# Kernel optimization log

Measured on AMD Instinct MI355X. Metric: run time of the kernel, lower is better.

Reference implementation:

```python
import jax, jax.numpy as jnp
import numpy as np

NT, NC = 100000, 25000
ETT, ECT = 800000, 400000
DIN_T, DIN_C = 64, 32
H, C = 4, 32
HID = H * C  # 128
SLOPE = 0.2  # GATConv LeakyReLU negative slope


def setup_inputs() -> dict:
    key = jax.random.key(0)
    ks = jax.random.split(key, 24)
    def p(i, shape, s=0.05):
        return jax.random.normal(ks[i], shape, dtype=jnp.float32) * s
    return {
        'x_target': jax.random.normal(ks[0], (NT, DIN_T), dtype=jnp.float32),
        'x_context': jax.random.normal(ks[1], (NC, DIN_C), dtype=jnp.float32),
        'edge_tt': jax.random.randint(ks[2], (2, ETT), 0, NT),
        'edge_ct_src': jax.random.randint(ks[3], (ECT,), 0, NC),
        'edge_ct_dst': jax.random.randint(ks[4], (ECT,), 0, NT),
        'W_pre_t': p(5, (DIN_T, HID)), 'b_pre_t': jnp.zeros((HID,), jnp.float32),
        'W_pre_c': p(6, (DIN_C, HID)), 'b_pre_c': jnp.zeros((HID,), jnp.float32),
        'W_sd': p(7, (HID, HID)), 'att_src_sd': p(8, (H, C)), 'att_dst_sd': p(9, (H, C)), 'b_sd': jnp.zeros((HID,), jnp.float32),
        'W_ds': p(10, (HID, HID)), 'att_src_ds': p(11, (H, C)), 'att_dst_ds': p(12, (H, C)), 'b_ds': jnp.zeros((HID,), jnp.float32),
        'W_ct_src': p(13, (HID, HID)), 'W_ct_dst': p(14, (HID, HID)), 'att_src_ct': p(15, (H, C)), 'att_dst_ct': p(16, (H, C)), 'b_ct': jnp.zeros((HID,), jnp.float32),
        'W_out': p(17, (HID, HID)), 'b_out': jnp.zeros((HID,), jnp.float32),
    }


def _gat(h_src, h_dst, att_s, att_d, src, dst, n_dst, bias):
    # h_src: [N_src,H,C] transformed src feats; h_dst: [N_dst,H,C]
    a_s = jnp.einsum('nhc,hc->nh', h_src, att_s)  # [N_src,H]
    a_d = jnp.einsum('nhc,hc->nh', h_dst, att_d)  # [N_dst,H]
    e = a_s[src] + a_d[dst]                        # [E,H]
    e = jnp.where(e > 0, e, SLOPE * e)             # LeakyReLU(0.2)
    m = jax.ops.segment_max(e, dst, num_segments=n_dst)  # stable softmax per dst
    ex = jnp.exp(e - m[dst])
    den = jax.ops.segment_sum(ex, dst, num_segments=n_dst)
    alpha = ex / den[dst]                          # [E,H]
    msg = h_src[src] * alpha[:, :, None]           # [E,H,C]
    out = jax.ops.segment_sum(msg, dst, num_segments=n_dst)
    return out.reshape(n_dst, H * C) + bias


def reference(x_target, x_context, edge_tt, edge_ct_src, edge_ct_dst,
              W_pre_t, b_pre_t, W_pre_c, b_pre_c,
              W_sd, att_src_sd, att_dst_sd, b_sd,
              W_ds, att_src_ds, att_dst_ds, b_ds,
              W_ct_src, W_ct_dst, att_src_ct, att_dst_ct, b_ct,
              W_out, b_out):
    # HeteroDictLinear pretransform + relu
    h_t = jax.nn.relu(x_target @ W_pre_t + b_pre_t)   # [NT,128]
    h_c = jax.nn.relu(x_context @ W_pre_c + b_pre_c)  # [NC,128]
    res = h_t
    # DirGATConv on (target,to,target): forward + reversed, each w/ self-loops
    loops = jnp.arange(NT)
    src_f = jnp.concatenate([edge_tt[0], loops]); dst_f = jnp.concatenate([edge_tt[1], loops])
    src_r = jnp.concatenate([edge_tt[1], loops]); dst_r = jnp.concatenate([edge_tt[0], loops])
    hs = (h_t @ W_sd).reshape(NT, H, C)
    out_sd = _gat(hs, hs, att_src_sd, att_dst_sd, src_f, dst_f, NT, b_sd)
    hd = (h_t @ W_ds).reshape(NT, H, C)
    out_ds = _gat(hd, hd, att_src_ds, att_dst_ds, src_r, dst_r, NT, b_ds)
    out_tt = 0.5 * out_sd + 0.5 * out_ds  # (1-alpha), alpha with alpha=0.5
    # bipartite GATConv on (context,to,target), no self loops
    hcs = (h_c @ W_ct_src).reshape(NC, H, C)
    htd = (h_t @ W_ct_dst).reshape(NT, H, C)
    out_ct = _gat(hcs, htd, att_src_ct, att_dst_ct, edge_ct_src, edge_ct_dst, NT, b_ct)
    # HeteroConv aggr='mean' over the two edge types hitting 'target'
    x = 0.5 * (out_tt + out_ct)
    x = jax.nn.relu(x + res)  # skip connection + relu
    return x @ W_out + b_out
```

## Files before the change

### kernel.cpp

```cpp
#include <hip/hip_runtime.h>
#include <cstdint>
#include <cstddef>

typedef unsigned short u16;
typedef unsigned int u32;

#define NT 100000
#define NC 25000
#define ETT 800000
#define ECT 400000
#define SLOPE 0.2f
#define LOG2E 1.4426950408889634f
#define OFFS (NT + 4)

#define NBK 782
#define NBLK 256
#define CHT ((ETT + NBLK - 1) / NBLK)
#define CHC ((ECT + NBLK - 1) / NBLK)
#define TOTC (3 * NBK * NBLK)
#define NSB ((TOTC + 4095) / 4096)
#define FILL_CAP 4096

#define PT_BLK ((NT + 63) / 64)
#define CT_BLK ((NC + 63) / 64)

typedef __attribute__((ext_vector_type(8))) short bf16x8;
typedef __attribute__((ext_vector_type(4))) float f32x4;

__device__ __forceinline__ u16 f2bf(float f) {
  u32 u = __float_as_uint(f);
  u32 r = (u >> 16) & 1u;
  return (u16)((u + 0x7fffu + r) >> 16);
}
__device__ __forceinline__ float lof(u32 p) { return __uint_as_float(p << 16); }
__device__ __forceinline__ float hif(u32 p) { return __uint_as_float(p & 0xffff0000u); }

__device__ __forceinline__ void compute_bpre(const int* __restrict__ bsum, int* s_bpre) {
  const int t = threadIdx.x;
  const int v = (t < NSB) ? bsum[t] : 0;
  s_bpre[t] = v;
  __syncthreads();
  for (int d = 1; d < 256; d <<= 1) {
    const int u = (t >= d) ? s_bpre[t - d] : 0;
    __syncthreads();
    s_bpre[t] += u;
    __syncthreads();
  }
  const int incl = s_bpre[t];
  __syncthreads();
  s_bpre[t] = incl - v;
  __syncthreads();
}

__global__ __launch_bounds__(256) void transform_hist_kernel(
    const int* __restrict__ tt_src, const int* __restrict__ tt_dst,
    const int* __restrict__ ect_d, int* __restrict__ cntblk,
    const float* __restrict__ Wsd, const float* __restrict__ AsSd, const float* __restrict__ AdSd,
    const float* __restrict__ Wds, const float* __restrict__ AsDs, const float* __restrict__ AdDs,
    const float* __restrict__ Wout,
    u16* __restrict__ bf_sd, u16* __restrict__ bf_ds, u16* __restrict__ bf_out,
    const float* __restrict__ Wcd, const float* __restrict__ attD,
    const float* __restrict__ bsd, const float* __restrict__ bds, const float* __restrict__ bct,
    float* __restrict__ cbias,
    const float* __restrict__ x_t, const float* __restrict__ Wpt, const float* __restrict__ bpt,
    u16* __restrict__ h_t, float* __restrict__ aD,
    const float* __restrict__ x_c, const float* __restrict__ Wpc, const float* __restrict__ bpc,
    const float* __restrict__ Wcs, const float* __restrict__ attS,
    u16* __restrict__ hc_bf, float* __restrict__ aS_c)
{
  __shared__ __align__(16) char smem[51200];
  const int t = threadIdx.x;

  if (blockIdx.x < NBLK) {
    int* h = (int*)smem;
    const int b = blockIdx.x;
    for (int i = t; i < 3 * NBK; i += 256) h[i] = 0;
    __syncthreads();
    const int lo = b * CHT, hi = min(lo + CHT, ETT);
    for (int i = lo + t; i < hi; i += 256) {
      atomicAdd(&h[tt_dst[i] >> 7], 1);
      atomicAdd(&h[NBK + (tt_src[i] >> 7)], 1);
    }
    const int lo2 = b * CHC, hi2 = min(lo2 + CHC, ECT);
    for (int i = lo2 + t; i < hi2; i += 256)
      atomicAdd(&h[2 * NBK + (ect_d[i] >> 7)], 1);
    __syncthreads();
    for (int i = t; i < 3 * NBK; i += 256)
      cntblk[(size_t)i * NBLK + b] = h[i];
    return;
  }

  const int b = blockIdx.x - NBLK;

  if (b < 4) {
    if (b == 3) {
      if (t < 128) cbias[t] = 0.25f * bsd[t] + 0.25f * bds[t] + 0.5f * bct[t];
      return;
    }
    float* fS = (float*)smem;
    float* fD = fS + 512;
    const float* W = (b == 0) ? Wsd : (b == 1) ? Wds : Wout;
    const float* As = (b == 0) ? AsSd : AsDs;
    const float* Ad = (b == 0) ? AdSd : AdDs;
    u16* out = (b == 0) ? bf_sd : (b == 1) ? bf_ds : bf_out;
    const int tiles = (b == 2) ? 8 : 9;
    if (b < 2) {
      if (t < 128) {
        for (int hh = 0; hh < 4; ++hh) {
          float s1 = 0.f, s2 = 0.f;
          for (int c = 0; c < 32; ++c) {
            const float wv = W[t * 128 + hh * 32 + c];
            s1 = fmaf(wv, As[hh * 32 + c], s1);
            s2 = fmaf(wv, Ad[hh * 32 + c], s2);
          }
          fS[t * 4 + hh] = s1 * LOG2E; fD[t * 4 + hh] = s2 * LOG2E;
        }
      }
      __syncthreads();
    }
    const int total = tiles * 4 * 64 * 8;
    for (int i = t; i < total; i += 256) {
// ... 34 lines not shown
    }
    const int rg = t >> 4;
    const int cg = t & 15;
    float acc[4][8];
    for (int r = 0; r < 4; ++r)
      for (int j = 0; j < 8; ++j)
        acc[r][j] = bpt[cg * 4 + (j & 3) + (j >> 2) * 64];
    for (int kc = 0; kc < 64; kc += 32) {
      for (int j = 0; j < 4; ++j) {
        const int idx = t + j * 256;
        const int k = idx >> 5, c4 = (idx & 31) * 4;
        *(float4*)&s_W[k][c4] = *(const float4*)(Wpt + (size_t)(kc + k) * 128 + c4);
      }
      __syncthreads();
#pragma unroll 8
      for (int k = 0; k < 32; ++k) {
        const float4 xa = *(const float4*)&s_xt[kc + k][rg * 4];
        const float4 w0 = *(const float4*)&s_W[k][cg * 4];
        const float4 w1 = *(const float4*)&s_W[k][cg * 4 + 64];
        const float xr[4] = {xa.x, xa.y, xa.z, xa.w};
        for (int r = 0; r < 4; ++r) {
          acc[r][0] = fmaf(xr[r], w0.x, acc[r][0]);
          acc[r][1] = fmaf(xr[r], w0.y, acc[r][1]);
          acc[r][2] = fmaf(xr[r], w0.z, acc[r][2]);
          acc[r][3] = fmaf(xr[r], w0.w, acc[r][3]);
          acc[r][4] = fmaf(xr[r], w1.x, acc[r][4]);
          acc[r][5] = fmaf(xr[r], w1.y, acc[r][5]);
          acc[r][6] = fmaf(xr[r], w1.z, acc[r][6]);
          acc[r][7] = fmaf(xr[r], w1.w, acc[r][7]);
        }
      }
      __syncthreads();
    }
    float4 fc0[2], fc1[2];
    fc0[0] = *(const float4*)&s_fold[(cg * 4 + 0) * 4];
    (void)fc0; (void)fc1;
    for (int r = 0; r < 4; ++r) {
      const int grow = row0 + rg * 4 + r;
      float v[8];
      for (int j = 0; j < 8; ++j) v[j] = fmaxf(acc[r][j], 0.f);
      float p0 = 0.f, p1 = 0.f, p2 = 0.f, p3 = 0.f;
      for (int j = 0; j < 8; ++j) {
        const int col = cg * 4 + (j & 3) + ((j >> 2) * 64);
        const float4 f4 = *(const float4*)&s_fold[col * 4];
        p0 = fmaf(v[j], f4.x, p0); p1 = fmaf(v[j], f4.y, p1);
        p2 = fmaf(v[j], f4.z, p2); p3 = fmaf(v[j], f4.w, p3);
      }
      if (grow < NT) {
        uint2 pk;
        pk.x = (u32)f2bf(v[0]) | ((u32)f2bf(v[1]) << 16);
        pk.y = (u32)f2bf(v[2]) | ((u32)f2bf(v[3]) << 16);
        *(uint2*)(h_t + (size_t)grow * 128 + cg * 4) = pk;
        pk.x = (u32)f2bf(v[4]) | ((u32)f2bf(v[5]) << 16);
        pk.y = (u32)f2bf(v[6]) | ((u32)f2bf(v[7]) << 16);
        *(uint2*)(h_t + (size_t)grow * 128 + cg * 4 + 64) = pk;
      }
      for (int m = 1; m < 16; m <<= 1) {
        p0 += __shfl_xor(p0, m); p1 += __shfl_xor(p1, m);
        p2 += __shfl_xor(p2, m); p3 += __shfl_xor(p3, m);
      }
      if (cg == 0 && grow < NT)
        *(float4*)(aD + (size_t)grow * 4) = make_float4(p0, p1, p2, p3);
    }
    return;
  }

  {
    float (*s_ht)[68]  = (float(*)[68])smem;
    float (*s_W2)[128] = (float(*)[128])(smem + 34816);
// ... 81 lines not shown
        __syncthreads();
      }
    }
    const int h2 = cg >> 3;
    const float4 at0 = *(const float4*)(attS + cg * 4);
    const float4 at1 = *(const float4*)(attS + cg * 4 + 64);
    for (int r = 0; r < 4; ++r) {
      const int grow = row0 + rg * 4 + r;
      float pa = acc2[r][0] * at0.x + acc2[r][1] * at0.y +
                 acc2[r][2] * at0.z + acc2[r][3] * at0.w;
      float pb = acc2[r][4] * at1.x + acc2[r][5] * at1.y +
                 acc2[r][6] * at1.z + acc2[r][7] * at1.w;
      if (grow < NC) {
        uint2 pk;
        pk.x = (u32)f2bf(acc2[r][0]) | ((u32)f2bf(acc2[r][1]) << 16);
        pk.y = (u32)f2bf(acc2[r][2]) | ((u32)f2bf(acc2[r][3]) << 16);
        *(uint2*)(hc_bf + (size_t)grow * 128 + cg * 4) = pk;
        pk.x = (u32)f2bf(acc2[r][4]) | ((u32)f2bf(acc2[r][5]) << 16);
        pk.y = (u32)f2bf(acc2[r][6]) | ((u32)f2bf(acc2[r][7]) << 16);
        *(uint2*)(hc_bf + (size_t)grow * 128 + cg * 4 + 64) = pk;
      }
      for (int m = 1; m < 8; m <<= 1) {
        pa += __shfl_xor(pa, m);
        pb += __shfl_xor(pb, m);
      }
      if ((cg & 7) == 0 && grow < NC) {
        aS_c[(size_t)grow * 4 + h2] = pa * LOG2E;
        aS_c[(size_t)grow * 4 + 2 + h2] = pb * LOG2E;
      }
    }
  }
}

__global__ __launch_bounds__(256) void scan2_blk_kernel(const int* __restrict__ in,
    int* __restrict__ out, int* __restrict__ bsum)
{
  const int t = threadIdx.x, b = blockIdx.x;
  const int idx = b * 4096 + t * 16;
  int v[16];
  int s = 0;
  if (idx < TOTC) {
#pragma unroll
    for (int q = 0; q < 4; ++q) {
      const int4 qq = *(const int4*)(in + idx + q * 4);
      v[q * 4 + 0] = s; s += qq.x;
      v[q * 4 + 1] = s; s += qq.y;
      v[q * 4 + 2] = s; s += qq.z;
      v[q * 4 + 3] = s; s += qq.w;
    }
  } else {
    for (int j = 0; j < 16; ++j) v[j] = 0;
  }
  __shared__ int sh[256];
  sh[t] = s;
  __syncthreads();
  for (int d = 1; d < 256; d <<= 1) {
    const int u = (t >= d) ? sh[t - d] : 0;
    __syncthreads();
    sh[t] += u;
    __syncthreads();
  }
  const int excl = (t == 0) ? 0 : sh[t - 1];
  if (idx < TOTC) {
#pragma unroll
    for (int q = 0; q < 4; ++q) {
      int4 qo;
      qo.x = excl + v[q * 4 + 0]; qo.y = excl + v[q * 4 + 1];
      qo.z = excl + v[q * 4 + 2]; qo.w = excl + v[q * 4 + 3];
      *(int4*)(out + idx + q * 4) = qo;
    }
  }
  if (t == 255) bsum[b] = sh[255];
}

__global__ __launch_bounds__(256) void bin_logits2_kernel(
    const int* __restrict__ tt_src, const int* __restrict__ tt_dst,
    const int* __restrict__ ect_s, const int* __restrict__ ect_d,
    const int* __restrict__ scanned, const int* __restrict__ bsum, u32* __restrict__ bin,
    const short* __restrict__ A, const short* __restrict__ Bsd, const short* __restrict__ Bds,
    u16* __restrict__ hs, float* __restrict__ aSsd, float* __restrict__ aDsd,
    u16* __restrict__ hd, float* __restrict__ aSds, float* __restrict__ aDds, int M)
{
  __shared__ __align__(16) float ldsf[4][16][148];
  const int t = threadIdx.x;

  if (blockIdx.x < NBLK) {
    int* cur = (int*)&ldsf[0][0][0];
    int* s_bpre = cur + 3 * NBK;
    compute_bpre(bsum, s_bpre);
    const int b = blockIdx.x;
    for (int i = t; i < 3 * NBK; i += 256) {
      const int idx = i * NBLK + b;
      cur[i] = scanned[idx] + s_bpre[idx >> 12];
    }
    __syncthreads();
    const int lo = b * CHT, hi = min(lo + CHT, ETT);
    for (int i = lo + t; i < hi; i += 256) {
      const int s = tt_src[i], d = tt_dst[i];
      int p = atomicAdd(&cur[d >> 7], 1);
      bin[p] = ((u32)(d & 127) << 17) | (u32)s;
      p = atomicAdd(&cur[NBK + (s >> 7)], 1);
      bin[p] = ((u32)(s & 127) << 17) | (u32)d;
    }
    const int lo2 = b * CHC, hi2 = min(lo2 + CHC, ECT);
    for (int i = lo2 + t; i < hi2; i += 256) {
      const int s = ect_s[i], d = ect_d[i];
      const int p = atomicAdd(&cur[2 * NBK + (d >> 7)], 1);
      bin[p] = ((u32)(d & 127) << 17) | (u32)s;
    }
    return;
  }

  float (*lds)[16][148] = ldsf;
  const int blk = blockIdx.x - NBLK;
  const int wv = t >> 6, lane = t & 63;
  const int quad = lane >> 4, l16 = lane & 15;
  const int row0 = blk * 64 + wv * 16;
  const int arow = min(row0 + l16, M - 1);
  const short* ap = A + (size_t)arow * 128 + quad * 8;
  bf16x8 af[4];
  for (int ks = 0; ks < 4; ++ks) af[ks] = *(const bf16x8*)(ap + ks * 32);
  const int row = row0 + l16;
  const int idx = lane & 7, rr = lane >> 3;
  for (int pass = 0; pass < 2; ++pass) {
    const short* B = pass ? Bds : Bsd;
    u16* outb = pass ? hd : hs;
    float* aS = pass ? aSds : aSsd;
    float* aD = pass ? aDds : aDsd;
    f32x4 acc[9];
    for (int ti = 0; ti < 9; ++ti) acc[ti] = (f32x4){0.f, 0.f, 0.f, 0.f};
    for (int ks = 0; ks < 4; ++ks)
      for (int ti = 0; ti < 9; ++ti) {
        const bf16x8 bf = *(const bf16x8*)(B + ((ti * 4 + ks) * 64 + lane) * 8);
        acc[ti] = __builtin_amdgcn_mfma_f32_16x16x32_bf16(af[ks], bf, acc[ti], 0, 0, 0);
      }
    for (int ti = 0; ti < 9; ++ti)
      for (int r = 0; r < 4; ++r)
        lds[wv][quad * 4 + r][ti * 16 + l16] = acc[ti][r];
    __syncthreads();
    if (row < M) {
      for (int g = 0; g < 8; ++g) {
        const f32x4 v = *(const f32x4*)&lds[wv][l16][g * 16 + quad * 4];
        uint2 pk;
        pk.x = (u32)f2bf(v[0]) | ((u32)f2bf(v[1]) << 16);
        pk.y = (u32)f2bf(v[2]) | ((u32)f2bf(v[3]) << 16);
        *(uint2*)(outb + (size_t)row * 128 + g * 16 + quad * 4) = pk;
      }
    }
    for (int p = 0; p < 2; ++p) {
      const int lr = p * 8 + rr;
      const int n = row0 + lr;
      if (n < M) {
        const float v = lds[wv][lr][128 + idx];
        if (idx < 4) aS[(size_t)n * 4 + idx] = v;
        else aD[(size_t)n * 4 + idx - 4] = v;
      }
    }
    __syncthreads();
  }
}

__global__ __launch_bounds__(256) void bucket_fill_kernel(const int* __restrict__ scanned,
    const int* __restrict__ bsum, const u32* __restrict__ bin,
    int* __restrict__ offs, int* __restrict__ big_el)
{
  __shared__ int s_cnt[128], s_exc[128], s_cur[128], s_bpre[256];
  __shared__ int s_el[FILL_CAP];
  const int t = threadIdx.x;
  compute_bpre(bsum, s_bpre);
  const int rel = blockIdx.x / NBK;
  const int bucket = blockIdx.x - rel * NBK;
  if (t < 128) s_cnt[t] = 0;
  const int bi = blockIdx.x * NBLK;
  const int base = scanned[bi] + s_bpre[bi >> 12];
  const int nxt = (blockIdx.x == 3 * NBK - 1)
                      ? (2 * ETT + ECT)
                      : scanned[bi + NBLK] + s_bpre[(bi + NBLK) >> 12];
  __syncthreads();
  const int size = nxt - base;
  for (int i = t; i < size; i += 256)
    atomicAdd(&s_cnt[bin[base + i] >> 17], 1);
  __syncthreads();
  if (t < 128) s_exc[t] = s_cnt[t];
  __syncthreads();
  for (int d = 1; d < 128; d <<= 1) {
    int v = 0;
    if (t < 128 && t >= d) v = s_exc[t - d];
    __syncthreads();
    if (t < 128) s_exc[t] += v;
    __syncthreads();
  }
  const int relbase = rel * ETT;
  const int obase = base - relbase;
  int* off_rel = offs + (size_t)rel * OFFS;
  const int node0 = bucket * 128;
  if (t < 128) {
    const int excl = s_exc[t] - s_cnt[t];
    s_cur[t] = excl;
    if (node0 + t < NT) off_rel[node0 + t] = obase + excl;
  }
  if (t == 0 && bucket == NBK - 1) off_rel[NT] = obase + size;
  __syncthreads();
  int* el_rel = big_el + relbase;
  if (size <= FILL_CAP) {
    for (int i = t; i < size; i += 256) {
      const u32 e = bin[base + i];
      const int pos = atomicAdd(&s_cur[e >> 17], 1);
      s_el[pos] = (int)(e & 0x1FFFFu);
    }
    __syncthreads();
    for (int i = t; i < size; i += 256)
      el_rel[obase + i] = s_el[i];
  } else {
    for (int i = t; i < size; i += 256) {
      const u32 e = bin[base + i];
      const int pos = atomicAdd(&s_cur[e >> 17], 1);
      el_rel[obase + pos] = (int)(e & 0x1FFFFu);
    }
  }
}

__global__ __launch_bounds__(256) void mfma_out_kernel(
    const short* __restrict__ A, const short* __restrict__ B,
    const float* __restrict__ bias, float* __restrict__ out, int M)
{
  __shared__ __align__(16) float lds[4][16][132];
  const int wv = threadIdx.x >> 6, lane = threadIdx.x & 63;
  const int quad = lane >> 4, l16 = lane & 15;
  const int row0 = blockIdx.x * 64 + wv * 16;
  const int arow = min(row0 + l16, M - 1);
  const short* ap = A + (size_t)arow * 128 + quad * 8;
  bf16x8 af[4];
  for (int ks = 0; ks < 4; ++ks) af[ks] = *(const bf16x8*)(ap + ks * 32);
  f32x4 acc[8];
  for (int t = 0; t < 8; ++t) acc[t] = (f32x4){0.f, 0.f, 0.f, 0.f};
  for (int ks = 0; ks < 4; ++ks)
    for (int t = 0; t < 8; ++t) {
      const bf16x8 bf = *(const bf16x8*)(B + ((t * 4 + ks) * 64 + lane) * 8);
      acc[t] = __builtin_amdgcn_mfma_f32_16x16x32_bf16(af[ks], bf, acc[t], 0, 0, 0);
    }
  for (int t = 0; t < 8; ++t)
    for (int r = 0; r < 4; ++r)
      lds[wv][quad * 4 + r][t * 16 + l16] = acc[t][r];
  __syncthreads();
  const int row = row0 + l16;
  if (row < M) {
    for (int g = 0; g < 8; ++g) {
      const int col = g * 16 + quad * 4;
      f32x4 v = *(const f32x4*)&lds[wv][l16][col];
      const f32x4 b4 = *(const f32x4*)(bias + col);
      v = v + b4;
      *(f32x4*)(out + (size_t)row * 128 + col) = v;
    }
  }
}

__device__ __forceinline__ void gat_pipe16(const int* __restrict__ off,
    const int* __restrict__ el, const float* __restrict__ aS, const float* __restrict__ aD,
    const u16* __restrict__ hb, int d, int h, int cb, int self_loop, float w,
    float* __restrict__ acc)
{
  const float ad = aD[(size_t)d * 4 + h];
  const int beg = off[d];
  const int m = off[d + 1] - beg;
  const int cnt = m + self_loop;
  if (cnt <= 0) return;
  float den = 0.f;
  float a0 = 0.f, a1 = 0.f, a2 = 0.f, a3 = 0.f, a4 = 0.f, a5 = 0.f, a6 = 0.f, a7 = 0.f;
  int sB = (1 < m) ? el[beg + 1] : d;
  {
    const int sA0 = (0 < m) ? el[beg] : d;
    float eA = aS[(size_t)sA0 * 4 + h];
    uint4 pA = *(const uint4*)(hb + (size_t)sA0 * 128 + cb);
    for (int k = 0; k < cnt; ++k) {
      const int sC = (k + 2 < m) ? el[beg + k + 2] : d;
      const float eB = aS[(size_t)sB * 4 + h];
      const uint4 pB = *(const uint4*)(hb + (size_t)sB * 128 + cb);
      float ea = eA + ad;
      ea = ea > 0.f ? ea : SLOPE * ea;
      const float ex = exp2f(ea);
      den += ex;
      a0 = fmaf(ex, lof(pA.x), a0); a1 = fmaf(ex, hif(pA.x), a1);
      a2 = fmaf(ex, lof(pA.y), a2); a3 = fmaf(ex, hif(pA.y), a3);
      a4 = fmaf(ex, lof(pA.z), a4); a5 = fmaf(ex, hif(pA.z), a5);
      a6 = fmaf(ex, lof(pA.w), a6); a7 = fmaf(ex, hif(pA.w), a7);
      eA = eB; pA = pB; sB = sC;
    }
  }
  const float s = w / den;
  acc[0] = fmaf(a0, s, acc[0]); acc[1] = fmaf(a1, s, acc[1]);
  acc[2] = fmaf(a2, s, acc[2]); acc[3] = fmaf(a3, s, acc[3]);
  acc[4] = fmaf(a4, s, acc[4]); acc[5] = fmaf(a5, s, acc[5]);
  acc[6] = fmaf(a6, s, acc[6]); acc[7] = fmaf(a7, s, acc[7]);
}

__global__ __launch_bounds__(256) void gather_all_kernel(
    const int* __restrict__ off_f, const int* __restrict__ el_f,
    const float* __restrict__ aS_sd, const float* __restrict__ aD_sd, const u16* __restrict__ hs,
    const int* __restrict__ off_r, const int* __restrict__ el_r,
    const float* __restrict__ aS_ds, const float* __restrict__ aD_ds, const u16* __restrict__ hd,
    const int* __restrict__ off_c, const int* __restrict__ el_c,
    const float* __restrict__ aS_ct, const float* __restrict__ aD_ct, const u16* __restrict__ hc,
    const u16* __restrict__ skip, const float* __restrict__ cbias, u16* __restrict__ x)
{
  const int d = blockIdx.x * 16 + (threadIdx.x >> 4);
  if (d >= NT) return;
  const int lg = threadIdx.x & 15;
  const int h = lg >> 2;
  const int cb = lg * 8;
  float acc[8];
  for (int i = 0; i < 8; ++i) acc[i] = 0.f;
  gat_pipe16(off_f, el_f, aS_sd, aD_sd, hs, d, h, cb, 1, 0.25f, acc);
  gat_pipe16(off_r, el_r, aS_ds, aD_ds, hd, d, h, cb, 1, 0.25f, acc);
  gat_pipe16(off_c, el_c, aS_ct, aD_ct, hc, d, h, cb, 0, 0.5f, acc);
  const uint4 sk = *(const uint4*)(skip + (size_t)d * 128 + cb);
  const float4 cb0 = *(const float4*)(cbias + cb);
  const float4 cb1 = *(const float4*)(cbias + cb + 4);
  const float o0 = fmaxf(acc[0] + cb0.x + lof(sk.x), 0.f);
  const float o1 = fmaxf(acc[1] + cb0.y + hif(sk.x), 0.f);
  const float o2 = fmaxf(acc[2] + cb0.z + lof(sk.y), 0.f);
  const float o3 = fmaxf(acc[3] + cb0.w + hif(sk.y), 0.f);
  const float o4 = fmaxf(acc[4] + cb1.x + lof(sk.z), 0.f);
  const float o5 = fmaxf(acc[5] + cb1.y + hif(sk.z), 0.f);
  const float o6 = fmaxf(acc[6] + cb1.z + lof(sk.w), 0.f);
  const float o7 = fmaxf(acc[7] + cb1.w + hif(sk.w), 0.f);
  uint4 r;
  r.x = (u32)f2bf(o0) | ((u32)f2bf(o1) << 16);
  r.y = (u32)f2bf(o2) | ((u32)f2bf(o3) << 16);
  r.z = (u32)f2bf(o4) | ((u32)f2bf(o5) << 16);
  r.w = (u32)f2bf(o6) | ((u32)f2bf(o7) << 16);
  *(uint4*)(x + (size_t)d * 128 + cb) = r;
}

extern "C" void kernel_launch(void* const* d_in, const int* in_sizes, int n_in,
                              void* d_out, int out_size, void* d_ws, size_t ws_size,
                              hipStream_t stream)
{
  const float* x_t   = (const float*)d_in[0];
  const float* x_c   = (const float*)d_in[1];
  const int*   e_tt  = (const int*)d_in[2];
  const int*   ect_s = (const int*)d_in[3];
  const int*   ect_d = (const int*)d_in[4];
  const float* Wpt = (const float*)d_in[5];   const float* bpt = (const float*)d_in[6];
  const float* Wpc = (const float*)d_in[7];   const float* bpc = (const float*)d_in[8];
  const float* Wsd = (const float*)d_in[9];   const float* As_sd = (const float*)d_in[10];
  const float* Ad_sd = (const float*)d_in[11]; const float* bsd = (const float*)d_in[12];
  const float* Wds = (const float*)d_in[13];  const float* As_ds = (const float*)d_in[14];
  const float* Ad_ds = (const float*)d_in[15]; const float* bds = (const float*)d_in[16];
  const float* Wcs = (const float*)d_in[17];  const float* Wcd = (const float*)d_in[18];
  const float* As_ct = (const float*)d_in[19]; const float* Ad_ct = (const float*)d_in[20];
  const float* bct = (const float*)d_in[21];
  const float* Wout = (const float*)d_in[22]; const float* bout = (const float*)d_in[23];

  char* p = (char*)d_ws;
  size_t off = 0;
  auto alloc = [&](size_t bytes) { char* r = p + off; off += (bytes + 255) & ~(size_t)255; return r; };
  u16* ht_bf   = (u16*)alloc((size_t)NT * 128 * 2);
  u16* hs_bf   = (u16*)alloc((size_t)NT * 128 * 2);
  u16* hd_bf   = (u16*)alloc((size_t)NT * 128 * 2);
  u16* hc_bf   = (u16*)alloc((size_t)NC * 128 * 2);
  u16* x_bf    = (u16*)alloc((size_t)NT * 128 * 2);
  float* aS_sd = (float*)alloc((size_t)NT * 4 * 4);
  float* aD_sd = (float*)alloc((size_t)NT * 4 * 4);
  float* aS_ds = (float*)alloc((size_t)NT * 4 * 4);
  float* aD_ds = (float*)alloc((size_t)NT * 4 * 4);
  float* aS_ct = (float*)alloc((size_t)NC * 4 * 4);
  float* aD_ct = (float*)alloc((size_t)NT * 4 * 4);
  int* cntblk  = (int*)alloc((size_t)TOTC * 4);
  int* scanned = (int*)alloc((size_t)TOTC * 4);
  u32* bin     = (u32*)alloc((size_t)(2 * ETT + ECT) * 4);
  int* big_el  = (int*)alloc((size_t)(2 * ETT + ECT) * 4);
  int* offs    = (int*)alloc((size_t)3 * OFFS * 4);
  int* bsum    = (int*)alloc((size_t)NSB * 4);
  float* cbias   = (float*)alloc(128 * 4);
  u16* bfrag_sd  = (u16*)alloc((size_t)9 * 4 * 64 * 8 * 2);
  u16* bfrag_ds  = (u16*)alloc((size_t)9 * 4 * 64 * 8 * 2);
  u16* bfrag_out = (u16*)alloc((size_t)8 * 4 * 64 * 8 * 2);

  int* off_f = offs;
  int* off_r = offs + OFFS;
  int* off_c = offs + 2 * OFFS;
  int* el_f = big_el;
  int* el_r = big_el + ETT;
  int* el_c = big_el + 2 * ETT;

  const int* tt_src = e_tt;
  const int* tt_dst = e_tt + ETT;

  const int gM = (NT + 63) / 64;

  transform_hist_kernel<<<NBLK + 4 + PT_BLK + CT_BLK, 256, 0, stream>>>(
      tt_src, tt_dst, ect_d, cntblk,
      Wsd, As_sd, Ad_sd, Wds, As_ds, Ad_ds, Wout,
      bfrag_sd, bfrag_ds, bfrag_out,
      Wcd, Ad_ct, bsd, bds, bct, cbias,
      x_t, Wpt, bpt, ht_bf, aD_ct,
      x_c, Wpc, bpc, Wcs, As_ct, hc_bf, aS_ct);

  scan2_blk_kernel<<<NSB, 256, 0, stream>>>(cntblk, scanned, bsum);

  bin_logits2_kernel<<<NBLK + gM, 256, 0, stream>>>(
      tt_src, tt_dst, ect_s, ect_d, scanned, bsum, bin,
      (const short*)ht_bf, (const short*)bfrag_sd, (const short*)bfrag_ds,
      hs_bf, aS_sd, aD_sd, hd_bf, aS_ds, aD_ds, NT);

  bucket_fill_kernel<<<3 * NBK, 256, 0, stream>>>(scanned, bsum, bin, offs, big_el);

  gather_all_kernel<<<(NT + 15) / 16, 256, 0, stream>>>(
      off_f, el_f, aS_sd, aD_sd, hs_bf,
      off_r, el_r, aS_ds, aD_ds, hd_bf,
      off_c, el_c, aS_ct, aD_ct, hc_bf,
      ht_bf, cbias, x_bf);

  mfma_out_kernel<<<gM, 256, 0, stream>>>((const short*)x_bf, (const short*)bfrag_out,
                                          bout, (float*)d_out, NT);
}
```

Before: 375.7 us.

## Replace bucketed two-pass CSR build with per-node degree count and direct scatter

The old CSR build did a per-block bucket histogram, a scan, a binning pass and a separate bucket_fill kernel that sorted each bucket in LDS. The new build counts per-node degree with global atomics, scans the node offsets and scatters edge ids straight into the CSR array using atomic cursors. This drops one kernel launch and the intermediate bin buffer, so the edge data is written once instead of twice. In exchange it relies on contended global atomics on random node addresses, needs an extra memset, and the order of edges within a node becomes nondeterministic.

```diff
diff --git a/kernel.cpp b/kernel.cpp
--- a/kernel.cpp
+++ b/kernel.cpp
@@ -13,13 +13,12 @@
 #define LOG2E 1.4426950408889634f
 #define OFFS (NT + 4)
 
-#define NBK 782
 #define NBLK 256
 #define CHT ((ETT + NBLK - 1) / NBLK)
 #define CHC ((ECT + NBLK - 1) / NBLK)
-#define TOTC (3 * NBK * NBLK)
-#define NSB ((TOTC + 4095) / 4096)
-#define FILL_CAP 4096
+#define NSB2 74
+#define SCN (NSB2 * 4096)
+#define PER (SCN / NBLK)
 
 #define PT_BLK ((NT + 63) / 64)
 #define CT_BLK ((NC + 63) / 64)
@@ -35,9 +34,10 @@
 __device__ __forceinline__ float lof(u32 p) { return __uint_as_float(p << 16); }
 __device__ __forceinline__ float hif(u32 p) { return __uint_as_float(p & 0xffff0000u); }
 
-__device__ __forceinline__ void compute_bpre(const int* __restrict__ bsum, int* s_bpre) {
+__device__ __forceinline__ void compute_bpre(const int* __restrict__ bsum,
+                                             int* s_bpre, int n) {
   const int t = threadIdx.x;
-  const int v = (t < NSB) ? bsum[t] : 0;
+  const int v = (t < n) ? bsum[t] : 0;
   s_bpre[t] = v;
   __syncthreads();
   for (int d = 1; d < 256; d <<= 1) {
@@ -52,9 +52,9 @@
   __syncthreads();
 }
 
-__global__ __launch_bounds__(256) void transform_hist_kernel(
+__global__ __launch_bounds__(256) void transform_count_kernel(
     const int* __restrict__ tt_src, const int* __restrict__ tt_dst,
-    const int* __restrict__ ect_d, int* __restrict__ cntblk,
+    const int* __restrict__ ect_d, int* __restrict__ deg,
     const float* __restrict__ Wsd, const float* __restrict__ AsSd, const float* __restrict__ AdSd,
     const float* __restrict__ Wds, const float* __restrict__ AsDs, const float* __restrict__ AdDs,
     const float* __restrict__ Wout,
@@ -72,21 +72,15 @@
   const int t = threadIdx.x;
 
   if (blockIdx.x < NBLK) {
-    int* h = (int*)smem;
     const int b = blockIdx.x;
-    for (int i = t; i < 3 * NBK; i += 256) h[i] = 0;
-    __syncthreads();
     const int lo = b * CHT, hi = min(lo + CHT, ETT);
     for (int i = lo + t; i < hi; i += 256) {
-      atomicAdd(&h[tt_dst[i] >> 7], 1);
-      atomicAdd(&h[NBK + (tt_src[i] >> 7)], 1);
+      atomicAdd(&deg[tt_dst[i]], 1);
+      atomicAdd(&deg[OFFS + tt_src[i]], 1);
     }
     const int lo2 = b * CHC, hi2 = min(lo2 + CHC, ECT);
     for (int i = lo2 + t; i < hi2; i += 256)
-      atomicAdd(&h[2 * NBK + (ect_d[i] >> 7)], 1);
-    __syncthreads();
-    for (int i = t; i < 3 * NBK; i += 256)
-      cntblk[(size_t)i * NBLK + b] = h[i];
+      atomicAdd(&deg[2 * OFFS + ect_d[i]], 1);
     return;
   }
 
@@ -187,9 +181,6 @@
       }
       __syncthreads();
     }
-    float4 fc0[2], fc1[2];
-    fc0[0] = *(const float4*)&s_fold[(cg * 4 + 0) * 4];
-    (void)fc0; (void)fc1;
     for (int r = 0; r < 4; ++r) {
       const int grow = row0 + rg * 4 + r;
       float v[8];
@@ -337,24 +328,20 @@
   }
 }
 
-__global__ __launch_bounds__(256) void scan2_blk_kernel(const int* __restrict__ in,
-    int* __restrict__ out, int* __restrict__ bsum)
+__global__ __launch_bounds__(256) void scan_nodes_kernel(const int* __restrict__ deg,
+    int* __restrict__ offs, int* __restrict__ cur, int* __restrict__ bsum)
 {
   const int t = threadIdx.x, b = blockIdx.x;
   const int idx = b * 4096 + t * 16;
   int v[16];
   int s = 0;
-  if (idx < TOTC) {
 #pragma unroll
-    for (int q = 0; q < 4; ++q) {
-      const int4 qq = *(const int4*)(in + idx + q * 4);
-      v[q * 4 + 0] = s; s += qq.x;
-      v[q * 4 + 1] = s; s += qq.y;
-      v[q * 4 + 2] = s; s += qq.z;
-      v[q * 4 + 3] = s; s += qq.w;
-    }
-  } else {
-    for (int j = 0; j < 16; ++j) v[j] = 0;
+  for (int q = 0; q < 4; ++q) {
+    const int4 qq = *(const int4*)(deg + idx + q * 4);
+    v[q * 4 + 0] = s; s += qq.x;
+    v[q * 4 + 1] = s; s += qq.y;
+    v[q * 4 + 2] = s; s += qq.z;
+    v[q * 4 + 3] = s; s += qq.w;
   }
   __shared__ int sh[256];
   sh[t] = s;
@@ -366,22 +353,22 @@
     __syncthreads();
   }
   const int excl = (t == 0) ? 0 : sh[t - 1];
-  if (idx < TOTC) {
 #pragma unroll
-    for (int q = 0; q < 4; ++q) {
-      int4 qo;
-      qo.x = excl + v[q * 4 + 0]; qo.y = excl + v[q * 4 + 1];
-      qo.z = excl + v[q * 4 + 2]; qo.w = excl + v[q * 4 + 3];
-      *(int4*)(out + idx + q * 4) = qo;
-    }
+  for (int q = 0; q < 4; ++q) {
+    int4 qo;
+    qo.x = excl + v[q * 4 + 0]; qo.y = excl + v[q * 4 + 1];
+    qo.z = excl + v[q * 4 + 2]; qo.w = excl + v[q * 4 + 3];
+    *(int4*)(offs + idx + q * 4) = qo;
+    *(int4*)(cur + idx + q * 4) = qo;
   }
   if (t == 255) bsum[b] = sh[255];
 }
 
-__global__ __launch_bounds__(256) void bin_logits2_kernel(
+__global__ __launch_bounds__(256) void scatter_logits2_kernel(
     const int* __restrict__ tt_src, const int* __restrict__ tt_dst,
     const int* __restrict__ ect_s, const int* __restrict__ ect_d,
-    const int* __restrict__ scanned, const int* __restrict__ bsum, u32* __restrict__ bin,
+    int* __restrict__ offs, int* __restrict__ cur, const int* __restrict__ bsum,
+    int* __restrict__ big_el,
     const short* __restrict__ A, const short* __restrict__ Bsd, const short* __restrict__ Bds,
     u16* __restrict__ hs, float* __restrict__ aSsd, float* __restrict__ aDsd,
     u16* __restrict__ hd, float* __restrict__ aSds, float* __restrict__ aDds, int M)
@@ -390,28 +377,26 @@
   const int t = threadIdx.x;
 
   if (blockIdx.x < NBLK) {
-    int* cur = (int*)&ldsf[0][0][0];
-    int* s_bpre = cur + 3 * NBK;
-    compute_bpre(bsum, s_bpre);
+    int* s_bpre = (int*)&ldsf[0][0][0];
+    compute_bpre(bsum, s_bpre, NSB2);
     const int b = blockIdx.x;
-    for (int i = t; i < 3 * NBK; i += 256) {
-      const int idx = i * NBLK + b;
-      cur[i] = scanned[idx] + s_bpre[idx >> 12];
-    }
-    __syncthreads();
+    for (int i = t; i < PER; i += 256) {
+      const int idx = b * PER + i;
+      offs[idx] += s_bpre[idx >> 12];
+    }
     const int lo = b * CHT, hi = min(lo + CHT, ETT);
     for (int i = lo + t; i < hi; i += 256) {
       const int s = tt_src[i], d = tt_dst[i];
-      int p = atomicAdd(&cur[d >> 7], 1);
-      bin[p] = ((u32)(d & 127) << 17) | (u32)s;
-      p = atomicAdd(&cur[NBK + (s >> 7)], 1);
-      bin[p] = ((u32)(s & 127) << 17) | (u32)d;
+      int p = atomicAdd(&cur[d], 1) + s_bpre[d >> 12];
+      big_el[p] = s;
+      p = atomicAdd(&cur[OFFS + s], 1) + s_bpre[(OFFS + s) >> 12];
+      big_el[p] = d;
     }
     const int lo2 = b * CHC, hi2 = min(lo2 + CHC, ECT);
     for (int i = lo2 + t; i < hi2; i += 256) {
-      const int s = ect_s[i], d = ect_d[i];
-      const int p = atomicAdd(&cur[2 * NBK + (d >> 7)], 1);
-      bin[p] = ((u32)(d & 127) << 17) | (u32)s;
+      const int dd = ect_d[i];
+      const int p = atomicAdd(&cur[2 * OFFS + dd], 1) + s_bpre[(2 * OFFS + dd) >> 12];
+      big_el[p] = ect_s[i];
     }
     return;
   }
@@ -462,66 +447,6 @@
       }
     }
     __syncthreads();
-  }
-}
-
-__global__ __launch_bounds__(256) void bucket_fill_kernel(const int* __restrict__ scanned,
-    const int* __restrict__ bsum, const u32* __restrict__ bin,
-    int* __restrict__ offs, int* __restrict__ big_el)
-{
-  __shared__ int s_cnt[128], s_exc[128], s_cur[128], s_bpre[256];
-  __shared__ int s_el[FILL_CAP];
-  const int t = threadIdx.x;
-  compute_bpre(bsum, s_bpre);
-  const int rel = blockIdx.x / NBK;
-  const int bucket = blockIdx.x - rel * NBK;
-  if (t < 128) s_cnt[t] = 0;
-  const int bi = blockIdx.x * NBLK;
-  const int base = scanned[bi] + s_bpre[bi >> 12];
-  const int nxt = (blockIdx.x == 3 * NBK - 1)
-                      ? (2 * ETT + ECT)
-                      : scanned[bi + NBLK] + s_bpre[(bi + NBLK) >> 12];
-  __syncthreads();
-  const int size = nxt - base;
-  for (int i = t; i < size; i += 256)
-    atomicAdd(&s_cnt[bin[base + i] >> 17], 1);
-  __syncthreads();
-  if (t < 128) s_exc[t] = s_cnt[t];
-  __syncthreads();
-  for (int d = 1; d < 128; d <<= 1) {
-    int v = 0;
-    if (t < 128 && t >= d) v = s_exc[t - d];
-    __syncthreads();
-    if (t < 128) s_exc[t] += v;
-    __syncthreads();
-  }
-  const int relbase = rel * ETT;
-  const int obase = base - relbase;
-  int* off_rel = offs + (size_t)rel * OFFS;
-  const int node0 = bucket * 128;
-  if (t < 128) {
-    const int excl = s_exc[t] - s_cnt[t];
-    s_cur[t] = excl;
-    if (node0 + t < NT) off_rel[node0 + t] = obase + excl;
-  }
-  if (t == 0 && bucket == NBK - 1) off_rel[NT] = obase + size;
-  __syncthreads();
-  int* el_rel = big_el + relbase;
-  if (size <= FILL_CAP) {
-    for (int i = t; i < size; i += 256) {
-      const u32 e = bin[base + i];
-      const int pos = atomicAdd(&s_cur[e >> 17], 1);
-      s_el[pos] = (int)(e & 0x1FFFFu);
-    }
-    __syncthreads();
-    for (int i = t; i < size; i += 256)
-      el_rel[obase + i] = s_el[i];
-  } else {
-    for (int i = t; i < size; i += 256) {
-      const u32 e = bin[base + i];
-      const int pos = atomicAdd(&s_cur[e >> 17], 1);
-      el_rel[obase + pos] = (int)(e & 0x1FFFFu);
-    }
   }
 }
 
@@ -671,50 +596,42 @@
   float* aD_ds = (float*)alloc((size_t)NT * 4 * 4);
   float* aS_ct = (float*)alloc((size_t)NC * 4 * 4);
   float* aD_ct = (float*)alloc((size_t)NT * 4 * 4);
-  int* cntblk  = (int*)alloc((size_t)TOTC * 4);
-  int* scanned = (int*)alloc((size_t)TOTC * 4);
-  u32* bin     = (u32*)alloc((size_t)(2 * ETT + ECT) * 4);
+  int* deg     = (int*)alloc((size_t)SCN * 4);
+  int* offs    = (int*)alloc((size_t)SCN * 4);
+  int* cur     = (int*)alloc((size_t)SCN * 4);
   int* big_el  = (int*)alloc((size_t)(2 * ETT + ECT) * 4);
-  int* offs    = (int*)alloc((size_t)3 * OFFS * 4);
-  int* bsum    = (int*)alloc((size_t)NSB * 4);
+  int* bsum    = (int*)alloc((size_t)NSB2 * 4);
   float* cbias   = (float*)alloc(128 * 4);
   u16* bfrag_sd  = (u16*)alloc((size_t)9 * 4 * 64 * 8 * 2);
   u16* bfrag_ds  = (u16*)alloc((size_t)9 * 4 * 64 * 8 * 2);
   u16* bfrag_out = (u16*)alloc((size_t)8 * 4 * 64 * 8 * 2);
 
-  int* off_f = offs;
-  int* off_r = offs + OFFS;
-  int* off_c = offs + 2 * OFFS;
-  int* el_f = big_el;
-  int* el_r = big_el + ETT;
-  int* el_c = big_el + 2 * ETT;
-
   const int* tt_src = e_tt;
   const int* tt_dst = e_tt + ETT;
 
   const int gM = (NT + 63) / 64;
 
-  transform_hist_kernel<<<NBLK + 4 + PT_BLK + CT_BLK, 256, 0, stream>>>(
-      tt_src, tt_dst, ect_d, cntblk,
+  hipMemsetAsync(deg, 0, (size_t)SCN * 4, stream);
+
+  transform_count_kernel<<<NBLK + 4 + PT_BLK + CT_BLK, 256, 0, stream>>>(
+      tt_src, tt_dst, ect_d, deg,
       Wsd, As_sd, Ad_sd, Wds, As_ds, Ad_ds, Wout,
       bfrag_sd, bfrag_ds, bfrag_out,
       Wcd, Ad_ct, bsd, bds, bct, cbias,
       x_t, Wpt, bpt, ht_bf, aD_ct,
       x_c, Wpc, bpc, Wcs, As_ct, hc_bf, aS_ct);
 
-  scan2_blk_kernel<<<NSB, 256, 0, stream>>>(cntblk, scanned, bsum);
-
-  bin_logits2_kernel<<<NBLK + gM, 256, 0, stream>>>(
-      tt_src, tt_dst, ect_s, ect_d, scanned, bsum, bin,
+  scan_nodes_kernel<<<NSB2, 256, 0, stream>>>(deg, offs, cur, bsum);
+
+  scatter_logits2_kernel<<<NBLK + gM, 256, 0, stream>>>(
+      tt_src, tt_dst, ect_s, ect_d, offs, cur, bsum, big_el,
       (const short*)ht_bf, (const short*)bfrag_sd, (const short*)bfrag_ds,
       hs_bf, aS_sd, aD_sd, hd_bf, aS_ds, aD_ds, NT);
 
-  bucket_fill_kernel<<<3 * NBK, 256, 0, stream>>>(scanned, bsum, bin, offs, big_el);
-
   gather_all_kernel<<<(NT + 15) / 16, 256, 0, stream>>>(
-      off_f, el_f, aS_sd, aD_sd, hs_bf,
-      off_r, el_r, aS_ds, aD_ds, hd_bf,
-      off_c, el_c, aS_ct, aD_ct, hc_bf,
+      offs, big_el, aS_sd, aD_sd, hs_bf,
+      offs + OFFS, big_el, aS_ds, aD_ds, hd_bf,
+      offs + 2 * OFFS, big_el, aS_ct, aD_ct, hc_bf,
       ht_bf, cbias, x_bf);
 
   mfma_out_kernel<<<gM, 256, 0, stream>>>((const short*)x_bf, (const short*)bfrag_out,
```

Measured after the change: 496.9 us. 32.3% more time.

## Split logits and output GEMM across kernels to overlap with fill and gather

Applied to the files above, without the earlier changes.

The logits MFMA work is split in half: the first half still runs alongside edge binning, and the second half now shares a launch with the bucket-fill blocks. The gather is also split at a row boundary. The second gather half runs in the same launch as the output GEMM for the first half of rows, and a final small kernel handles the remaining output rows. The intent is to fill idle CUs during the memory-bound and atomic-heavy phases with independent compute, cutting tail effects and launch gaps. The cost is extra kernel-body complexity, and co-resident blocks of different kinds may contend for LDS and occupancy.

```diff
diff --git a/kernel.cpp b/kernel.cpp
--- a/kernel.cpp
+++ b/kernel.cpp
@@ -23,6 +23,14 @@
 
 #define PT_BLK ((NT + 63) / 64)
 #define CT_BLK ((NC + 63) / 64)
+
+#define LROWS1 782
+#define LROWS2 781
+#define GOH 50048
+#define G1BLK (GOH / 16)
+#define G2BLK ((NT - GOH + 15) / 16)
+#define OB1 (GOH / 64)
+#define OB2 ((NT - GOH + 63) / 64)
 
 typedef __attribute__((ext_vector_type(8))) short bf16x8;
 typedef __attribute__((ext_vector_type(4))) float f32x4;
@@ -187,9 +195,6 @@
       }
       __syncthreads();
     }
-    float4 fc0[2], fc1[2];
-    fc0[0] = *(const float4*)&s_fold[(cg * 4 + 0) * 4];
-    (void)fc0; (void)fc1;
     for (int r = 0; r < 4; ++r) {
       const int grow = row0 + rg * 4 + r;
       float v[8];
@@ -378,49 +383,15 @@
   if (t == 255) bsum[b] = sh[255];
 }
 
-__global__ __launch_bounds__(256) void bin_logits2_kernel(
-    const int* __restrict__ tt_src, const int* __restrict__ tt_dst,
-    const int* __restrict__ ect_s, const int* __restrict__ ect_d,
-    const int* __restrict__ scanned, const int* __restrict__ bsum, u32* __restrict__ bin,
+__device__ __forceinline__ void logits2_body(float (*lds)[16][148], int blk, int rbase,
     const short* __restrict__ A, const short* __restrict__ Bsd, const short* __restrict__ Bds,
     u16* __restrict__ hs, float* __restrict__ aSsd, float* __restrict__ aDsd,
     u16* __restrict__ hd, float* __restrict__ aSds, float* __restrict__ aDds, int M)
 {
-  __shared__ __align__(16) float ldsf[4][16][148];
   const int t = threadIdx.x;
-
-  if (blockIdx.x < NBLK) {
-    int* cur = (int*)&ldsf[0][0][0];
-    int* s_bpre = cur + 3 * NBK;
-    compute_bpre(bsum, s_bpre);
-    const int b = blockIdx.x;
-    for (int i = t; i < 3 * NBK; i += 256) {
-      const int idx = i * NBLK + b;
-      cur[i] = scanned[idx] + s_bpre[idx >> 12];
-    }
-    __syncthreads();
-    const int lo = b * CHT, hi = min(lo + CHT, ETT);
-    for (int i = lo + t; i < hi; i += 256) {
-      const int s = tt_src[i], d = tt_dst[i];
-      int p = atomicAdd(&cur[d >> 7], 1);
-      bin[p] = ((u32)(d & 127) << 17) | (u32)s;
-      p = atomicAdd(&cur[NBK + (s >> 7)], 1);
-      bin[p] = ((u32)(s & 127) << 17) | (u32)d;
-    }
-    const int lo2 = b * CHC, hi2 = min(lo2 + CHC, ECT);
-    for (int i = lo2 + t; i < hi2; i += 256) {
-      const int s = ect_s[i], d = ect_d[i];
-      const int p = atomicAdd(&cur[2 * NBK + (d >> 7)], 1);
-      bin[p] = ((u32)(d & 127) << 17) | (u32)s;
-    }
-    return;
-  }
-
-  float (*lds)[16][148] = ldsf;
-  const int blk = blockIdx.x - NBLK;
   const int wv = t >> 6, lane = t & 63;
   const int quad = lane >> 4, l16 = lane & 15;
-  const int row0 = blk * 64 + wv * 16;
+  const int row0 = rbase + blk * 64 + wv * 16;
   const int arow = min(row0 + l16, M - 1);
   const short* ap = A + (size_t)arow * 128 + quad * 8;
   bf16x8 af[4];
@@ -465,90 +436,145 @@
   }
 }
 
-__global__ __launch_bounds__(256) void bucket_fill_kernel(const int* __restrict__ scanned,
-    const int* __restrict__ bsum, const u32* __restrict__ bin,
-    int* __restrict__ offs, int* __restrict__ big_el)
-{
-  __shared__ int s_cnt[128], s_exc[128], s_cur[128], s_bpre[256];
-  __shared__ int s_el[FILL_CAP];
+__global__ __launch_bounds__(256) void bin_logits2_kernel(
+    const int* __restrict__ tt_src, const int* __restrict__ tt_dst,
+    const int* __restrict__ ect_s, const int* __restrict__ ect_d,
+    const int* __restrict__ scanned, const int* __restrict__ bsum, u32* __restrict__ bin,
+    const short* __restrict__ A, const short* __restrict__ Bsd, const short* __restrict__ Bds,
+    u16* __restrict__ hs, float* __restrict__ aSsd, float* __restrict__ aDsd,
+    u16* __restrict__ hd, float* __restrict__ aSds, float* __restrict__ aDds, int M)
+{
+  __shared__ __align__(16) float ldsf[4][16][148];
   const int t = threadIdx.x;
-  compute_bpre(bsum, s_bpre);
-  const int rel = blockIdx.x / NBK;
-  const int bucket = blockIdx.x - rel * NBK;
-  if (t < 128) s_cnt[t] = 0;
-  const int bi = blockIdx.x * NBLK;
-  const int base = scanned[bi] + s_bpre[bi >> 12];
-  const int nxt = (blockIdx.x == 3 * NBK - 1)
-                      ? (2 * ETT + ECT)
-                      : scanned[bi + NBLK] + s_bpre[(bi + NBLK) >> 12];
-  __syncthreads();
-  const int size = nxt - base;
-  for (int i = t; i < size; i += 256)
-    atomicAdd(&s_cnt[bin[base + i] >> 17], 1);
-  __syncthreads();
-  if (t < 128) s_exc[t] = s_cnt[t];
-  __syncthreads();
-  for (int d = 1; d < 128; d <<= 1) {
-    int v = 0;
-    if (t < 128 && t >= d) v = s_exc[t - d];
-    __syncthreads();
-    if (t < 128) s_exc[t] += v;
-    __syncthreads();
-  }
-  const int relbase = rel * ETT;
-  const int obase = base - relbase;
-  int* off_rel = offs + (size_t)rel * OFFS;
-  const int node0 = bucket * 128;
-  if (t < 128) {
-    const int excl = s_exc[t] - s_cnt[t];
-    s_cur[t] = excl;
-    if (node0 + t < NT) off_rel[node0 + t] = obase + excl;
-  }
-  if (t == 0 && bucket == NBK - 1) off_rel[NT] = obase + size;
-  __syncthreads();
-  int* el_rel = big_el + relbase;
-  if (size <= FILL_CAP) {
-    for (int i = t; i < size; i += 256) {
-      const u32 e = bin[base + i];
-      const int pos = atomicAdd(&s_cur[e >> 17], 1);
-      s_el[pos] = (int)(e & 0x1FFFFu);
-    }
-    __syncthreads();
+
+  if (blockIdx.x < NBLK) {
+    int* cur = (int*)&ldsf[0][0][0];
+    int* s_bpre = cur + 3 * NBK;
+    compute_bpre(bsum, s_bpre);
+    const int b = blockIdx.x;
+    for (int i = t; i < 3 * NBK; i += 256) {
+      const int idx = i * NBLK + b;
+      cur[i] = scanned[idx] + s_bpre[idx >> 12];
+    }
+    __syncthreads();
+    const int lo = b * CHT, hi = min(lo + CHT, ETT);
+    for (int i = lo + t; i < hi; i += 256) {
+      const int s = tt_src[i], d = tt_dst[i];
+      int p = atomicAdd(&cur[d >> 7], 1);
+      bin[p] = ((u32)(d & 127) << 17) | (u32)s;
+      p = atomicAdd(&cur[NBK + (s >> 7)], 1);
+      bin[p] = ((u32)(s & 127) << 17) | (u32)d;
+    }
+    const int lo2 = b * CHC, hi2 = min(lo2 + CHC, ECT);
+    for (int i = lo2 + t; i < hi2; i += 256) {
+      const int s = ect_s[i], d = ect_d[i];
+      const int p = atomicAdd(&cur[2 * NBK + (d >> 7)], 1);
+      bin[p] = ((u32)(d & 127) << 17) | (u32)s;
+    }
+    return;
+  }
+  logits2_body(ldsf, blockIdx.x - NBLK, 0, A, Bsd, Bds,
+               hs, aSsd, aDsd, hd, aSds, aDds, M);
+}
+
+__global__ __launch_bounds__(256) void fill_logits2_kernel(
+    const int* __restrict__ scanned, const int* __restrict__ bsum, const u32* __restrict__ bin,
+    int* __restrict__ offs, int* __restrict__ big_el,
+    const short* __restrict__ A, const short* __restrict__ Bsd, const short* __restrict__ Bds,
+    u16* __restrict__ hs, float* __restrict__ aSsd, float* __restrict__ aDsd,
+    u16* __restrict__ hd, float* __restrict__ aSds, float* __restrict__ aDds, int M)
+{
+  __shared__ __align__(16) float ldsf[4][16][148];
+  const int t = threadIdx.x;
+
+  if (blockIdx.x < 3 * NBK) {
+    int* base0 = (int*)&ldsf[0][0][0];
+    int* s_cnt = base0;
+    int* s_exc = base0 + 128;
+    int* s_cur = base0 + 256;
+    int* s_bpre = base0 + 384;
+    int* s_el = base0 + 640;
+    compute_bpre(bsum, s_bpre);
+    const int rel = blockIdx.x / NBK;
+    const int bucket = blockIdx.x - rel * NBK;
+    if (t < 128) s_cnt[t] = 0;
+    const int bi = blockIdx.x * NBLK;
+    const int base = scanned[bi] + s_bpre[bi >> 12];
+    const int nxt = (blockIdx.x == 3 * NBK - 1)
+                        ? (2 * ETT + ECT)
+                        : scanned[bi + NBLK] + s_bpre[(bi + NBLK) >> 12];
+    __syncthreads();
+    const int size = nxt - base;
     for (int i = t; i < size; i += 256)
-      el_rel[obase + i] = s_el[i];
-  } else {
-    for (int i = t; i < size; i += 256) {
-      const u32 e = bin[base + i];
-      const int pos = atomicAdd(&s_cur[e >> 17], 1);
-      el_rel[obase + pos] = (int)(e & 0x1FFFFu);
-    }
-  }
-}
-
-__global__ __launch_bounds__(256) void mfma_out_kernel(
+      atomicAdd(&s_cnt[bin[base + i] >> 17], 1);
+    __syncthreads();
+    if (t < 128) s_exc[t] = s_cnt[t];
+    __syncthreads();
+    for (int d = 1; d < 128; d <<= 1) {
+      int v = 0;
+      if (t < 128 && t >= d) v = s_exc[t - d];
+      __syncthreads();
+      if (t < 128) s_exc[t] += v;
+      __syncthreads();
+    }
+    const int relbase = rel * ETT;
+    const int obase = base - relbase;
+    int* off_rel = offs + (size_t)rel * OFFS;
+    const int node0 = bucket * 128;
+    if (t < 128) {
+      const int excl = s_exc[t] - s_cnt[t];
+      s_cur[t] = excl;
+      if (node0 + t < NT) off_rel[node0 + t] = obase + excl;
+    }
+    if (t == 0 && bucket == NBK - 1) off_rel[NT] = obase + size;
+    __syncthreads();
+    int* el_rel = big_el + relbase;
+    if (size <= FILL_CAP) {
+      for (int i = t; i < size; i += 256) {
+        const u32 e = bin[base + i];
+        const int pos = atomicAdd(&s_cur[e >> 17], 1);
+        s_el[pos] = (int)(e & 0x1FFFFu);
+      }
+      __syncthreads();
+      for (int i = t; i < size; i += 256)
+        el_rel[obase + i] = s_el[i];
+    } else {
+      for (int i = t; i < size; i += 256) {
+        const u32 e = bin[base + i];
+        const int pos = atomicAdd(&s_cur[e >> 17], 1);
+        el_rel[obase + pos] = (int)(e & 0x1FFFFu);
+      }
+    }
+    return;
+  }
+  logits2_body(ldsf, blockIdx.x - 3 * NBK, GOH, A, Bsd, Bds,
+               hs, aSsd, aDsd, hd, aSds, aDds, M);
+}
+
+__device__ __forceinline__ void mfma_out_body(float (*lds)[16][132], int row0,
     const short* __restrict__ A, const short* __restrict__ B,
     const float* __restrict__ bias, float* __restrict__ out, int M)
 {
-  __shared__ __align__(16) float lds[4][16][132];
-  const int wv = threadIdx.x >> 6, lane = threadIdx.x & 63;
+  const int t = threadIdx.x;
+  const int wv = t >> 6, lane = t & 63;
   const int quad = lane >> 4, l16 = lane & 15;
-  const int row0 = blockIdx.x * 64 + wv * 16;
-  const int arow = min(row0 + l16, M - 1);
+  const int r0 = row0 + wv * 16;
+  const int arow = min(r0 + l16, M - 1);
   const short* ap = A + (size_t)arow * 128 + quad * 8;
   bf16x8 af[4];
   for (int ks = 0; ks < 4; ++ks) af[ks] = *(const bf16x8*)(ap + ks * 32);
   f32x4 acc[8];
-  for (int t = 0; t < 8; ++t) acc[t] = (f32x4){0.f, 0.f, 0.f, 0.f};
+  for (int ti = 0; ti < 8; ++ti) acc[ti] = (f32x4){0.f, 0.f, 0.f, 0.f};
   for (int ks = 0; ks < 4; ++ks)
-    for (int t = 0; t < 8; ++t) {
-      const bf16x8 bf = *(const bf16x8*)(B + ((t * 4 + ks) * 64 + lane) * 8);
-      acc[t] = __builtin_amdgcn_mfma_f32_16x16x32_bf16(af[ks], bf, acc[t], 0, 0, 0);
-    }
-  for (int t = 0; t < 8; ++t)
+    for (int ti = 0; ti < 8; ++ti) {
+      const bf16x8 bf = *(const bf16x8*)(B + ((ti * 4 + ks) * 64 + lane) * 8);
+      acc[ti] = __builtin_amdgcn_mfma_f32_16x16x32_bf16(af[ks], bf, acc[ti], 0, 0, 0);
+    }
+  for (int ti = 0; ti < 8; ++ti)
     for (int r = 0; r < 4; ++r)
-      lds[wv][quad * 4 + r][t * 16 + l16] = acc[t][r];
+      lds[wv][quad * 4 + r][ti * 16 + l16] = acc[ti][r];
   __syncthreads();
-  const int row = row0 + l16;
+  const int row = r0 + l16;
   if (row < M) {
     for (int g = 0; g < 8; ++g) {
       const int col = g * 16 + quad * 4;
@@ -558,6 +584,14 @@
       *(f32x4*)(out + (size_t)row * 128 + col) = v;
     }
   }
+}
+
+__global__ __launch_bounds__(256) void mfma_out_kernel(
+    const short* __restrict__ A, const short* __restrict__ B,
+    const float* __restrict__ bias, float* __restrict__ out, int rbase, int M)
+{
+  __shared__ __align__(16) float lds[4][16][132];
+  mfma_out_body(lds, rbase + blockIdx.x * 64, A, B, bias, out, M);
 }
 
 __device__ __forceinline__ void gat_pipe16(const int* __restrict__ off,
@@ -599,7 +633,7 @@
   acc[6] = fmaf(a6, s, acc[6]); acc[7] = fmaf(a7, s, acc[7]);
 }
 
-__global__ __launch_bounds__(256) void gather_all_kernel(
+__device__ __forceinline__ void gather_body(int d,
     const int* __restrict__ off_f, const int* __restrict__ el_f,
     const float* __restrict__ aS_sd, const float* __restrict__ aD_sd, const u16* __restrict__ hs,
     const int* __restrict__ off_r, const int* __restrict__ el_r,
@@ -608,8 +642,6 @@
     const float* __restrict__ aS_ct, const float* __restrict__ aD_ct, const u16* __restrict__ hc,
     const u16* __restrict__ skip, const float* __restrict__ cbias, u16* __restrict__ x)
 {
-  const int d = blockIdx.x * 16 + (threadIdx.x >> 4);
-  if (d >= NT) return;
   const int lg = threadIdx.x & 15;
   const int h = lg >> 2;
   const int cb = lg * 8;
@@ -637,6 +669,42 @@
   *(uint4*)(x + (size_t)d * 128 + cb) = r;
 }
 
+__global__ __launch_bounds__(256) void gather_all_kernel(
+    const int* __restrict__ off_f, const int* __restrict__ el_f,
+    const float* __restrict__ aS_sd, const float* __restrict__ aD_sd, const u16* __restrict__ hs,
+    const int* __restrict__ off_r, const int* __restrict__ el_r,
+    const float* __restrict__ aS_ds, const float* __restrict__ aD_ds, const u16* __restrict__ hd,
+    const int* __restrict__ off_c, const int* __restrict__ el_c,
+    const float* __restrict__ aS_ct, const float* __restrict__ aD_ct, const u16* __restrict__ hc,
+    const u16* __restrict__ skip, const float* __restrict__ cbias, u16* __restrict__ x)
+{
+  const int d = blockIdx.x * 16 + (threadIdx.x >> 4);
+  if (d >= NT) return;
+  gather_body(d, off_f, el_f, aS_sd, aD_sd, hs, off_r, el_r, aS_ds, aD_ds, hd,
+              off_c, el_c, aS_ct, aD_ct, hc, skip, cbias, x);
+}
+
+__global__ __launch_bounds__(256) void gather_out_kernel(
+    const int* __restrict__ off_f, const int* __restrict__ el_f,
+    const float* __restrict__ aS_sd, const float* __restrict__ aD_sd, const u16* __restrict__ hs,
+    const int* __restrict__ off_r, const int* __restrict__ el_r,
+    const float* __restrict__ aS_ds, const float* __restrict__ aD_ds, const u16* __restrict__ hd,
+    const int* __restrict__ off_c, const int* __restrict__ el_c,
+    const float* __restrict__ aS_ct, const float* __restrict__ aD_ct, const u16* __restrict__ hc,
+    const u16* __restrict__ skip, const float* __restrict__ cbias, u16* __restrict__ x,
+    const short* __restrict__ B, const float* __restrict__ bias, float* __restrict__ out, int M)
+{
+  __shared__ __align__(16) float lds[4][16][132];
+  if (blockIdx.x < G2BLK) {
+    const int d = GOH + blockIdx.x * 16 + (threadIdx.x >> 4);
+    if (d >= NT) return;
+    gather_body(d, off_f, el_f, aS_sd, aD_sd, hs, off_r, el_r, aS_ds, aD_ds, hd,
+                off_c, el_c, aS_ct, aD_ct, hc, skip, cbias, x);
+    return;
+  }
+  mfma_out_body(lds, (blockIdx.x - G2BLK) * 64, (const short*)x, B, bias, out, M);
+}
+
 extern "C" void kernel_launch(void* const* d_in, const int* in_sizes, int n_in,
                               void* d_out, int out_size, void* d_ws, size_t ws_size,
                               hipStream_t stream)
@@ -692,8 +760,6 @@
   const int* tt_src = e_tt;
   const int* tt_dst = e_tt + ETT;
 
-  const int gM = (NT + 63) / 64;
-
   transform_hist_kernel<<<NBLK + 4 + PT_BLK + CT_BLK, 256, 0, stream>>>(
       tt_src, tt_dst, ect_d, cntblk,
       Wsd, As_sd, Ad_sd, Wds, As_ds, Ad_ds, Wout,
@@ -704,19 +770,29 @@
 
   scan2_blk_kernel<<<NSB, 256, 0, stream>>>(cntblk, scanned, bsum);
 
-  bin_logits2_kernel<<<NBLK + gM, 256, 0, stream>>>(
+  bin_logits2_kernel<<<NBLK + LROWS1, 256, 0, stream>>>(
       tt_src, tt_dst, ect_s, ect_d, scanned, bsum, bin,
       (const short*)ht_bf, (const short*)bfrag_sd, (const short*)bfrag_ds,
       hs_bf, aS_sd, aD_sd, hd_bf, aS_ds, aD_ds, NT);
 
-  bucket_fill_kernel<<<3 * NBK, 256, 0, stream>>>(scanned, bsum, bin, offs, big_el);
-
-  gather_all_kernel<<<(NT + 15) / 16, 256, 0, stream>>>(
+  fill_logits2_kernel<<<3 * NBK + LROWS2, 256, 0, stream>>>(
+      scanned, bsum, bin, offs, big_el,
+      (const short*)ht_bf, (const short*)bfrag_sd, (const short*)bfrag_ds,
+      hs_bf, aS_sd, aD_sd, hd_bf, aS_ds, aD_ds, NT);
+
+  gather_all_kernel<<<G1BLK, 256, 0, stream>>>(
       off_f, el_f, aS_sd, aD_sd, hs_bf,
       off_r, el_r, aS_ds, aD_ds, hd_bf,
       off_c, el_c, aS_ct, aD_ct, hc_bf,
       ht_bf, cbias, x_bf);
 
-  mfma_out_kernel<<<gM, 256, 0, stream>>>((const short*)x_bf, (const short*)bfrag_out,
-                                          bout, (float*)d_out, NT);
-}
+  gather_out_kernel<<<G2BLK + OB1, 256, 0, stream>>>(
+      off_f, el_f, aS_sd, aD_sd, hs_bf,
+      off_r, el_r, aS_ds, aD_ds, hd_bf,
+      off_c, el_c, aS_ct, aD_ct, hc_bf,
+      ht_bf, cbias, x_bf,
+      (const short*)bfrag_out, bout, (float*)d_out, NT);
+
+  mfma_out_kernel<<<OB2, 256, 0, stream>>>((const short*)x_bf, (const short*)bfrag_out,
+                                           bout, (float*)d_out, GOH, NT);
+}
```

After: 409.7 us. 1.09x slower.
